# Performance work log

Hardware: AMD Instinct MI355X
Metric: run time of the kernel (lower is better)

Reference implementation:

```python
import jax, jax.numpy as jnp
import numpy as np

N_NODES = 50000


def _degree_norm(idx, n):
    # D^{-1/2} with degree clamped to >= 1 (DGL GraphConv norm='both')
    deg = jax.ops.segment_sum(jnp.ones(idx.shape[0], jnp.float32), idx, num_segments=n)
    return jax.lax.rsqrt(jnp.maximum(deg, 1.0))


def gcn_layer(src, dst, x, W, b, relu):
    n = x.shape[0]
    norm_src = _degree_norm(src, n)  # out-degree norm on source side
    norm_dst = _degree_norm(dst, n)  # in-degree norm on destination side
    # apply weight first (in_feats >= out_feats path in DGL): [N, F] @ [F, O]
    h = x @ W
    h = h * norm_src[:, None]
    # SpMM aggregation: gather source rows, scatter-add into destinations
    agg = jax.ops.segment_sum(h[src], dst, num_segments=n)
    out = agg * norm_dst[:, None] + b
    return jax.nn.relu(out) if relu else out


def setup_inputs() -> dict:
    key = jax.random.key(0)
    k1, k2, k3, k4, k5, k6, k7 = jax.random.split(key, 7)
    in_f, hid_f, out_f = 64, 64, 16
    n_edges = 800000
    features = jax.random.normal(k1, (N_NODES, in_f), jnp.float32)
    src = jax.random.randint(k2, (n_edges,), 0, N_NODES, jnp.int32)
    dst = jax.random.randint(k3, (n_edges,), 0, N_NODES, jnp.int32)
    # Glorot-uniform init as in DGL GraphConv
    lim1 = float(np.sqrt(6.0 / (in_f + hid_f)))
    lim2 = float(np.sqrt(6.0 / (hid_f + out_f)))
    W1 = jax.random.uniform(k4, (in_f, hid_f), jnp.float32, -lim1, lim1)
    b1 = jnp.zeros((hid_f,), jnp.float32)
    W2 = jax.random.uniform(k5, (hid_f, out_f), jnp.float32, -lim2, lim2)
    b2 = jnp.zeros((out_f,), jnp.float32)
    return {"features": features, "src": src, "dst": dst,
            "W1": W1, "b1": b1, "W2": W2, "b2": b2}


def reference(features, src, dst, W1, b1, W2, b2):
    # layer 0: GraphConv(in->hidden) with relu; dropout is identity (eval mode)
    h = gcn_layer(src, dst, features, W1, b1, relu=True)
    # layer 1: GraphConv(hidden->out), no activation
    h = gcn_layer(src, dst, h, W2, b2, relu=False)
    return h
```

## Files before the change

### kernel.cpp

```cpp
#include <hip/hip_runtime.h>
#include <hip/hip_fp16.h>

#define FEAT1 64
#define FEAT2 16
#define MAXB 5120
#define FCAP 4608
#define EB   200

typedef _Float16 f16x8 __attribute__((ext_vector_type(8)));
typedef _Float16 f16x4 __attribute__((ext_vector_type(4)));
typedef float f32x4 __attribute__((ext_vector_type(4)));
typedef float f32x2 __attribute__((ext_vector_type(2)));

#define DPP_ADD(x, ctrl) \
    ((x) + __int_as_float(__builtin_amdgcn_update_dpp(0, __float_as_int(x), (ctrl), 0xf, 0xf, true)))


__global__ __launch_bounds__(256) void gemm_part(const float* __restrict__ X,
                                                 const float* __restrict__ W1,
                                                 const int* __restrict__ src,
                                                 const int* __restrict__ dst,
                                                 int* __restrict__ gcurS,
                                                 int* __restrict__ gcurD,
                                                 unsigned int* __restrict__ packD,
                                                 unsigned char* __restrict__ srcLow,
                                                 unsigned char* __restrict__ h1,
                                                 int N, int E, int chunkE) {
    __shared__ __attribute__((aligned(16))) char smem[18432];
    const int tid = threadIdx.x, bid = blockIdx.x;
    const int gemmBlks = (N + 127) >> 7;

    if (bid < gemmBlks) {
        _Float16* sWt = (_Float16*)smem;
        _Float16* sTileAll = (_Float16*)(smem + 9216);
        for (int i = tid; i < 4096; i += 256) {
            int k = i >> 6, n = i & 63;
            sWt[n * 72 + k] = (_Float16)W1[i];
        }
        __syncthreads();
        int wave = tid >> 6, lane = tid & 63;
        int m = lane & 15, quad = lane >> 4;
        f16x8 bfrag[4][2];
#pragma unroll
        for (int nt = 0; nt < 4; nt++)
#pragma unroll
            for (int kit = 0; kit < 2; kit++)
                bfrag[nt][kit] = *(const f16x8*)&sWt[(nt * 16 + m) * 72 + kit * 32 + quad * 8];
        _Float16* tile = sTileAll + wave * (16 * 72);
        int row_blk = bid * 128;
#pragma unroll
        for (int t = 0; t < 2; t++) {
            int row0 = row_blk + wave * 32 + t * 16;
            int row = row0 + m;
            bool inb = row < N;
            f32x4 acc[4] = {{0.f,0.f,0.f,0.f},{0.f,0.f,0.f,0.f},{0.f,0.f,0.f,0.f},{0.f,0.f,0.f,0.f}};
#pragma unroll
            for (int kit = 0; kit < 2; kit++) {
                f16x8 afrag;
                if (inb) {
                    const float4* xp = (const float4*)(X + (size_t)row * 64 + kit * 32 + quad * 8);
                    float4 x0 = xp[0], x1 = xp[1];
                    afrag[0] = (_Float16)x0.x; afrag[1] = (_Float16)x0.y;
                    afrag[2] = (_Float16)x0.z; afrag[3] = (_Float16)x0.w;
                    afrag[4] = (_Float16)x1.x; afrag[5] = (_Float16)x1.y;
                    afrag[6] = (_Float16)x1.z; afrag[7] = (_Float16)x1.w;
                } else {
#pragma unroll
                    for (int j = 0; j < 8; j++) afrag[j] = (_Float16)0.f;
                }
#pragma unroll
                for (int nt = 0; nt < 4; nt++)
                    acc[nt] = __builtin_amdgcn_mfma_f32_16x16x32_f16(afrag, bfrag[nt][kit], acc[nt], 0, 0, 0);
            }
#pragma unroll
            for (int reg = 0; reg < 4; reg++) {
                int r = quad * 4 + reg;
#pragma unroll
                for (int nt = 0; nt < 4; nt++)
                    tile[r * 72 + nt * 16 + m] = (_Float16)acc[nt][reg];
            }
            __syncthreads();
            int rr = lane >> 2, g = lane & 3;
            f16x8 p0 = *(const f16x8*)&tile[rr * 72 + g * 16];
            f16x8 p1 = *(const f16x8*)&tile[rr * 72 + g * 16 + 8];
            int orow = row0 + rr;
            if (orow < N) {
                int a, b;
                uint4 wv;
                a = __builtin_amdgcn_cvt_pk_fp8_f32((float)p0[0], (float)p0[1], 0, false);
                b = __builtin_amdgcn_cvt_pk_fp8_f32((float)p0[2], (float)p0[3], a, true);
                wv.x = (unsigned)b;
                a = __builtin_amdgcn_cvt_pk_fp8_f32((float)p0[4], (float)p0[5], 0, false);
                b = __builtin_amdgcn_cvt_pk_fp8_f32((float)p0[6], (float)p0[7], a, true);
                wv.y = (unsigned)b;
                a = __builtin_amdgcn_cvt_pk_fp8_f32((float)p1[0], (float)p1[1], 0, false);
                b = __builtin_amdgcn_cvt_pk_fp8_f32((float)p1[2], (float)p1[3], a, true);
                wv.z = (unsigned)b;
                a = __builtin_amdgcn_cvt_pk_fp8_f32((float)p1[4], (float)p1[5], 0, false);
                b = __builtin_amdgcn_cvt_pk_fp8_f32((float)p1[6], (float)p1[7], a, true);
                wv.w = (unsigned)b;
                *(uint4*)(h1 + (size_t)orow * 64 + g * 16) = wv;
            }
            __syncthreads();
        }
    } else {
        int* hS = (int*)smem;
        int* hD = (int*)(smem + 1024);
        int* bS = (int*)(smem + 2048);
        int* bD = (int*)(smem + 3072);
        int eb = bid - gemmBlks;
        hS[tid] = 0; hD[tid] = 0;
        __syncthreads();
        int e0 = eb * chunkE;
        int e1 = min(e0 + chunkE, E);
        int nq = (e1 - e0) >> 2;
        for (int q = tid; q < nq; q += 256) {
            int e = e0 + q * 4;
            int4 s4 = *(const int4*)(src + e);
            int4 d4 = *(const int4*)(dst + e);
            atomicAdd(&hS[s4.x >> 8], 1); atomicAdd(&hS[s4.y >> 8], 1);
            atomicAdd(&hS[s4.z >> 8], 1); atomicAdd(&hS[s4.w >> 8], 1);
            atomicAdd(&hD[d4.x >> 8], 1); atomicAdd(&hD[d4.y >> 8], 1);
            atomicAdd(&hD[d4.z >> 8], 1); atomicAdd(&hD[d4.w >> 8], 1);
        }
        for (int e = e0 + nq * 4 + tid; e < e1; e += 256) {
            atomicAdd(&hS[src[e] >> 8], 1);
            atomicAdd(&hD[dst[e] >> 8], 1);
        }
        __syncthreads();
        int cS = hS[tid], cD = hD[tid];
        bS[tid] = cS ? atomicAdd(&gcurS[tid], cS) : 0;
        bD[tid] = cD ? atomicAdd(&gcurD[tid], cD) : 0;
        __syncthreads();
        hS[tid] = bS[tid];
        hD[tid] = bD[tid];
        __syncthreads();
        for (int q = tid; q < nq; q += 256) {
            int e = e0 + q * 4;
            int4 s4 = *(const int4*)(src + e);
            int4 d4 = *(const int4*)(dst + e);
            int ss[4] = {s4.x, s4.y, s4.z, s4.w};
            int dd[4] = {d4.x, d4.y, d4.z, d4.w};
#pragma unroll
            for (int k = 0; k < 4; k++) {
                int s = ss[k], d = dd[k];
                int pD = atomicAdd(&hD[d >> 8], 1);
                packD[(size_t)(d >> 8) * MAXB + pD] = ((unsigned)(d & 255) << 16) | (unsigned)s;
                int pS = atomicAdd(&hS[s >> 8], 1);
                srcLow[(size_t)(s >> 8) * MAXB + pS] = (unsigned char)(s & 255);
            }
        }
        for (int e = e0 + nq * 4 + tid; e < e1; e += 256) {
            int s = src[e], d = dst[e];
            int pD = atomicAdd(&hD[d >> 8], 1);
            packD[(size_t)(d >> 8) * MAXB + pD] = ((unsigned)(d & 255) << 16) | (unsigned)s;
            int pS = atomicAdd(&hS[s >> 8], 1);
            srcLow[(size_t)(s >> 8) * MAXB + pS] = (unsigned char)(s & 255);
        }
    }
}


__global__ __launch_bounds__(256) void fine_both(const unsigned int* __restrict__ packD,
                                                 const int* __restrict__ gcurD,
                                                 unsigned short* __restrict__ sorted_src,
                                                 int2* __restrict__ oc,
                                                 float* __restrict__ norm_dst,
                                                 const unsigned char* __restrict__ srcLow,
                                                 const int* __restrict__ gcurS,
                                                 float* __restrict__ norm_src, int N) {
    __shared__ int hist[256], cur[256], wtot[4];
    __shared__ unsigned int ecache[FCAP];
    int tid = threadIdx.x;
    if (blockIdx.x < 256) {
        int b = blockIdx.x;
        int n = gcurD[b];
        int base = b * MAXB;
        hist[tid] = 0;
        __syncthreads();
        for (int i = tid; i < n; i += 256) {
            unsigned p = packD[base + i];
            if (i < FCAP) ecache[i] = p;
            atomicAdd(&hist[p >> 16], 1);
        }
        __syncthreads();
        int v = hist[tid];
        int lane = tid & 63, wid = tid >> 6;
        int x = v;
#pragma unroll
        for (int off = 1; off < 64; off <<= 1) {
            int t = __shfl_up(x, off, 64);
            if (lane >= off) x += t;
        }
        if (lane == 63) wtot[wid] = x;
        __syncthreads();
        int add = 0;
#pragma unroll
        for (int w2 = 0; w2 < 3; w2++) add += (w2 < wid) ? wtot[w2] : 0;
        int excl = x + add - v;
        cur[tid] = excl;
        int node = b * 256 + tid;
        if (node < N) {
            oc[node] = make_int2(base + excl, v);
            norm_dst[node] = rsqrtf(fmaxf((float)v, 1.0f));
        }
        __syncthreads();
        for (int i = tid; i < n; i += 256) {
            unsigned p = (i < FCAP) ? ecache[i] : packD[base + i];
            int pos = atomicAdd(&cur[p >> 16], 1);
            sorted_src[base + pos] = (unsigned short)(p & 0xFFFFu);
        }
    } else {
        int b = blockIdx.x - 256;
        int n = gcurS[b];
        int base = b * MAXB;
        hist[tid] = 0;
        __syncthreads();
        for (int i = tid; i < n; i += 256) atomicAdd(&hist[srcLow[base + i]], 1);
        __syncthreads();
        int node = b * 256 + tid;
        if (node < N) norm_src[node] = rsqrtf(fmaxf((float)hist[tid], 1.0f));
    }
}


__global__ __launch_bounds__(256) void agg1_fused(const unsigned char* __restrict__ h1,
                                                  const unsigned short* __restrict__ sorted_src,
                                                  const int2* __restrict__ oc,
                                                  const float* __restrict__ norm_dst,
                                                  const float* __restrict__ norm_src,
                                                  const float* __restrict__ b1,
                                                  const float* __restrict__ W2,
                                                  __half* __restrict__ h2, int N, int nwaves) {
    int tid = threadIdx.x;
    int wave = tid >> 6, lane = tid & 63;
    int e_off = lane >> 3;
    int fg = lane & 7;
    float w2r[8][2], b1r[8];
#pragma unroll
    for (int k = 0; k < 8; k++) {
        float2 t = *(const float2*)(W2 + (size_t)(fg * 8 + k) * 16 + 2 * e_off);
        w2r[k][0] = t.x; w2r[k][1] = t.y;
        b1r[k] = b1[fg * 8 + k];
    }
    for (int row = blockIdx.x * 4 + wave; row < N; row += nwaves) {
        int2 sc = oc[row];
        int start = sc.x, c = sc.y;
        float nd = norm_dst[row];
        f32x2 acc2[4] = {{0.f,0.f},{0.f,0.f},{0.f,0.f},{0.f,0.f}};
        for (int j = 0; j < c; j += 8) {
            int je = j + e_off;
            if (je < c) {
                int s = sorted_src[start + je];
                float nse = norm_src[s];
                uint2 wv = *(const uint2*)(h1 + (size_t)s * 64 + fg * 8);
                acc2[0] += __builtin_amdgcn_cvt_pk_f32_fp8((int)wv.x, false) * nse;
                acc2[1] += __builtin_amdgcn_cvt_pk_f32_fp8((int)wv.x, true)  * nse;
                acc2[2] += __builtin_amdgcn_cvt_pk_f32_fp8((int)wv.y, false) * nse;
                acc2[3] += __builtin_amdgcn_cvt_pk_f32_fp8((int)wv.y, true)  * nse;
            }
        }
        float acc[8] = {acc2[0][0], acc2[0][1], acc2[1][0], acc2[1][1],
                        acc2[2][0], acc2[2][1], acc2[3][0], acc2[3][1]};
#pragma unroll
        for (int k = 0; k < 8; k++) acc[k] = DPP_ADD(acc[k], 0x128);
#pragma unroll
        for (int m = 16; m <= 32; m <<= 1)
#pragma unroll
            for (int k = 0; k < 8; k++) acc[k] += __shfl_xor(acc[k], m);
        float p0 = 0.f, p1 = 0.f;
#pragma unroll
        for (int k = 0; k < 8; k++) {
            float t = fmaxf(acc[k] * nd + b1r[k], 0.f);
            p0 += t * w2r[k][0];
            p1 += t * w2r[k][1];
        }
        p0 = DPP_ADD(p0, 0xB1);
        p1 = DPP_ADD(p1, 0xB1);
        p0 = DPP_ADD(p0, 0x4E);
        p1 = DPP_ADD(p1, 0x4E);
        p0 += __shfl_xor(p0, 4);
        p1 += __shfl_xor(p1, 4);
        if (fg == 0) {
            float ns = norm_src[row];
            ((__half2*)((_Float16*)h2 + (size_t)row * 16))[e_off] =
                __floats2half2_rn(p0 * ns, p1 * ns);
        }
    }
}


__global__ __launch_bounds__(256) void agg2_kernel(const __half* __restrict__ h2,
                                                   const unsigned short* __restrict__ sorted_src,
                                                   const int2* __restrict__ oc,
                                                   const float* __restrict__ norm_dst,
                                                   const float* __restrict__ b2,
                                                   float* __restrict__ out, int N, int nwaves) {
    int tid = threadIdx.x;
    int wave = tid >> 6, lane = tid & 63;
    int e_off = lane >> 2;
    int fg = lane & 3;
    float b2r[4];
#pragma unroll
    for (int k = 0; k < 4; k++) b2r[k] = b2[fg * 4 + k];
    const _Float16* h2p = (const _Float16*)h2;
    for (int row = blockIdx.x * 4 + wave; row < N; row += nwaves) {
        int2 sc = oc[row];
        int start = sc.x, c = sc.y;
        f32x2 acc2[2] = {{0.f,0.f},{0.f,0.f}};
        for (int j = 0; j < c; j += 16) {
            int je = j + e_off;
            if (je < c) {
                int s = sorted_src[start + je];
                f16x4 v = *(const f16x4*)(h2p + (size_t)s * 16 + fg * 4);
                f32x2 f0 = {(float)v[0], (float)v[1]};
                f32x2 f1 = {(float)v[2], (float)v[3]};
                acc2[0] += f0;
                acc2[1] += f1;
            }
        }
        float acc[4] = {acc2[0][0], acc2[0][1], acc2[1][0], acc2[1][1]};
#pragma unroll
        for (int k = 0; k < 4; k++) acc[k] += __shfl_xor(acc[k], 4);
#pragma unroll
        for (int k = 0; k < 4; k++) acc[k] = DPP_ADD(acc[k], 0x128);
#pragma unroll
        for (int m = 16; m <= 32; m <<= 1)
#pragma unroll
            for (int k = 0; k < 4; k++) acc[k] += __shfl_xor(acc[k], m);
        if (e_off == 0) {
            float nd = norm_dst[row];
            float4 o;
            o.x = acc[0] * nd + b2r[0];
            o.y = acc[1] * nd + b2r[1];
            o.z = acc[2] * nd + b2r[2];
            o.w = acc[3] * nd + b2r[3];
            ((float4*)(out + (size_t)row * 16))[fg] = o;
        }
    }
}

extern "C" void kernel_launch(void* const* d_in, const int* in_sizes, int n_in,
                              void* d_out, int out_size, void* d_ws, size_t ws_size,
                              hipStream_t stream) {
    const float* X  = (const float*)d_in[0];
    const int* src  = (const int*)d_in[1];
    const int* dst  = (const int*)d_in[2];
    const float* W1 = (const float*)d_in[3];
    const float* b1 = (const float*)d_in[4];
    const float* W2 = (const float*)d_in[5];
    const float* b2 = (const float*)d_in[6];
    float* out = (float*)d_out;

    const int N = in_sizes[0] / FEAT1;
    const int E = in_sizes[1];
    const int chunkE = (((E + EB - 1) / EB) + 3) & ~3;

    char* w = (char*)d_ws;
    int* gcurS = (int*)w;        w += 1024;
    int* gcurD = (int*)w;        w += 1024;
    unsigned int* packD = (unsigned int*)w;          w += (size_t)256 * MAXB * 4;
    unsigned char* srcLow = (unsigned char*)w;       w += (size_t)256 * MAXB;
    unsigned short* sorted_src = (unsigned short*)w; w += (size_t)256 * MAXB * 2;
    w = (char*)(((size_t)w + 7) & ~(size_t)7);
    int2* oc = (int2*)w;         w += (size_t)N * 8;
    float* norm_src = (float*)w; w += (size_t)N * 4;
    float* norm_dst = (float*)w; w += (size_t)N * 4;
    unsigned char* h1 = (unsigned char*)w; w += (size_t)N * 64;
    __half* h2 = (__half*)w;     w += (size_t)N * 16 * 2;

    hipMemsetAsync(d_ws, 0, 2048, stream);

    const int gemmBlks = (N + 127) / 128;
    gemm_part<<<gemmBlks + EB, 256, 0, stream>>>(X, W1, src, dst, gcurS, gcurD,
                                                 packD, srcLow, h1, N, E, chunkE);
    fine_both<<<512, 256, 0, stream>>>(packD, gcurD, sorted_src, oc, norm_dst,
                                       srcLow, gcurS, norm_src, N);
    const int nblk1 = 4096;
    agg1_fused<<<nblk1, 256, 0, stream>>>(h1, sorted_src, oc, norm_dst, norm_src,
                                          b1, W2, h2, N, nblk1 * 4);
    const int nblk2 = 3072;
    agg2_kernel<<<nblk2, 256, 0, stream>>>(h2, sorted_src, oc, norm_dst, b2, out, N, nblk2 * 4);
}
```

Measured before the change: 149.9 us.

## Map one row per 4-lane group in agg2 and enlarge edge-binning block count

The second aggregation kernel now assigns each destination row to a 4-lane group (16 rows per wave) that walks all of that row's edges serially, instead of spreading one row's edges across a whole wave. This removes the cross-lane shuffle/DPP reduction and the wasted lanes on low-degree rows, at the cost of load imbalance and divergence within a wave when degrees differ. The grid is sized to cover N rows exactly. Separately, the number of edge-partition blocks EB rises from 200 to 320, changing the chunking in the binning phase.

```diff
diff --git a/kernel.cpp b/kernel.cpp
--- a/kernel.cpp
+++ b/kernel.cpp
@@ -5,7 +5,7 @@
 #define FEAT2 16
 #define MAXB 5120
 #define FCAP 4608
-#define EB   200
+#define EB   320
 
 typedef _Float16 f16x8 __attribute__((ext_vector_type(8)));
 typedef _Float16 f16x4 __attribute__((ext_vector_type(4)));
@@ -295,48 +295,34 @@
                                                    const int2* __restrict__ oc,
                                                    const float* __restrict__ norm_dst,
                                                    const float* __restrict__ b2,
-                                                   float* __restrict__ out, int N, int nwaves) {
+                                                   float* __restrict__ out, int N, int rows_step) {
     int tid = threadIdx.x;
     int wave = tid >> 6, lane = tid & 63;
-    int e_off = lane >> 2;
+    int grp = lane >> 2;
     int fg = lane & 3;
     float b2r[4];
 #pragma unroll
     for (int k = 0; k < 4; k++) b2r[k] = b2[fg * 4 + k];
     const _Float16* h2p = (const _Float16*)h2;
-    for (int row = blockIdx.x * 4 + wave; row < N; row += nwaves) {
+    for (int row = (blockIdx.x * 4 + wave) * 16 + grp; row < N; row += rows_step) {
         int2 sc = oc[row];
         int start = sc.x, c = sc.y;
         f32x2 acc2[2] = {{0.f,0.f},{0.f,0.f}};
-        for (int j = 0; j < c; j += 16) {
-            int je = j + e_off;
-            if (je < c) {
-                int s = sorted_src[start + je];
-                f16x4 v = *(const f16x4*)(h2p + (size_t)s * 16 + fg * 4);
-                f32x2 f0 = {(float)v[0], (float)v[1]};
-                f32x2 f1 = {(float)v[2], (float)v[3]};
-                acc2[0] += f0;
-                acc2[1] += f1;
-            }
-        }
-        float acc[4] = {acc2[0][0], acc2[0][1], acc2[1][0], acc2[1][1]};
-#pragma unroll
-        for (int k = 0; k < 4; k++) acc[k] += __shfl_xor(acc[k], 4);
-#pragma unroll
-        for (int k = 0; k < 4; k++) acc[k] = DPP_ADD(acc[k], 0x128);
-#pragma unroll
-        for (int m = 16; m <= 32; m <<= 1)
-#pragma unroll
-            for (int k = 0; k < 4; k++) acc[k] += __shfl_xor(acc[k], m);
-        if (e_off == 0) {
-            float nd = norm_dst[row];
-            float4 o;
-            o.x = acc[0] * nd + b2r[0];
-            o.y = acc[1] * nd + b2r[1];
-            o.z = acc[2] * nd + b2r[2];
-            o.w = acc[3] * nd + b2r[3];
-            ((float4*)(out + (size_t)row * 16))[fg] = o;
-        }
+        for (int j = 0; j < c; j++) {
+            int s = sorted_src[start + j];
+            f16x4 v = *(const f16x4*)(h2p + (size_t)s * 16 + fg * 4);
+            f32x2 f0 = {(float)v[0], (float)v[1]};
+            f32x2 f1 = {(float)v[2], (float)v[3]};
+            acc2[0] += f0;
+            acc2[1] += f1;
+        }
+        float nd = norm_dst[row];
+        float4 o;
+        o.x = acc2[0][0] * nd + b2r[0];
+        o.y = acc2[0][1] * nd + b2r[1];
+        o.z = acc2[1][0] * nd + b2r[2];
+        o.w = acc2[1][1] * nd + b2r[3];
+        ((float4*)(out + (size_t)row * 16))[fg] = o;
     }
 }
 
@@ -379,6 +365,7 @@
     const int nblk1 = 4096;
     agg1_fused<<<nblk1, 256, 0, stream>>>(h1, sorted_src, oc, norm_dst, norm_src,
                                           b1, W2, h2, N, nblk1 * 4);
-    const int nblk2 = 3072;
-    agg2_kernel<<<nblk2, 256, 0, stream>>>(h2, sorted_src, oc, norm_dst, b2, out, N, nblk2 * 4);
-}
+    const int nblk2 = (N + 63) / 64;
+    agg2_kernel<<<nblk2, 256, 0, stream>>>(h2, sorted_src, oc, norm_dst, b2, out,
+                                           N, nblk2 * 64);
+}
```

New measurement: 150.0 us. Within noise of the previous version (+0.1%).
